# Performance work log

Hardware: AMD Instinct MI355X
Metric: run time of the kernel (lower is better)

Reference implementation:

```python
import jax, jax.numpy as jnp
import numpy as np

B, S, D, H = 2, 2048, 512, 8
DK = D // H
MASK_VALUE = -1e9


def setup_inputs() -> dict:
    key = jax.random.key(0)
    ks = jax.random.split(key, 12)
    scale = 1.0 / np.sqrt(D)
    inp = {
        "query": jax.random.normal(ks[0], (B, S, D), jnp.float32),
        "key": jax.random.normal(ks[1], (B, S, D), jnp.float32),
        "value": jax.random.normal(ks[2], (B, S, D), jnp.float32),
        # causal mask, broadcastable over batch and heads
        "mask": jnp.tril(jnp.ones((S, S), jnp.int32))[None, None, :, :],
        "Wq": jax.random.normal(ks[3], (D, D), jnp.float32) * scale,
        "bq": jax.random.normal(ks[4], (D,), jnp.float32) * scale,
        "Wk": jax.random.normal(ks[5], (D, D), jnp.float32) * scale,
        "bk": jax.random.normal(ks[6], (D,), jnp.float32) * scale,
        "Wv": jax.random.normal(ks[7], (D, D), jnp.float32) * scale,
        "bv": jax.random.normal(ks[8], (D,), jnp.float32) * scale,
        "Wo": jax.random.normal(ks[9], (D, D), jnp.float32) * scale,
        "bo": jax.random.normal(ks[10], (D,), jnp.float32) * scale,
    }
    return inp


def reference(query, key, value, mask, Wq, bq, Wk, bk, Wv, bv, Wo, bo):
    # linear projections (torch Linear: x @ W.T + b)
    q = query @ Wq.T + bq
    k = key @ Wk.T + bk
    v = value @ Wv.T + bv
    # split heads: [B,S,D] -> [B,H,S,DK]
    q = q.reshape(B, S, H, DK).transpose(0, 2, 1, 3)
    k = k.reshape(B, S, H, DK).transpose(0, 2, 1, 3)
    v = v.reshape(B, S, H, DK).transpose(0, 2, 1, 3)
    # scaled dot-product attention with explicit [B,H,S,S] score matrix
    scores = jnp.einsum("bhqd,bhkd->bhqk", q, k) / jnp.sqrt(jnp.float32(DK))
    scores = jnp.where(mask == 0, jnp.float32(MASK_VALUE), scores)
    attn = jax.nn.softmax(scores, axis=-1)
    x = jnp.einsum("bhqk,bhkd->bhqd", attn, v)
    # merge heads: [B,H,S,DK] -> [B,S,D]
    x = x.transpose(0, 2, 1, 3).reshape(B, S, D)
    return x @ Wo.T + bo
```

## Files before the change

### kernel.cpp

```cpp
#include <hip/hip_runtime.h>
#include <hip/hip_bf16.h>

#define B_   2
#define S_   2048
#define D_   512
#define H_   8
#define DK_  64
#define M_   (B_*S_)

typedef float  floatx4 __attribute__((ext_vector_type(4)));
typedef __bf16 bf16x8  __attribute__((ext_vector_type(8)));

#define MFMA16x16x32(a,b,c) __builtin_amdgcn_mfma_f32_16x16x32_bf16((a),(b),(c),0,0,0)

static __device__ __forceinline__ void load_lds16(const void* g, void* l) {
  __builtin_amdgcn_global_load_lds(
      (const __attribute__((address_space(1))) void*)g,
      (__attribute__((address_space(3))) void*)l,
      16, 0, 0);
}

static __device__ __forceinline__ bf16x8 cvt8(float4 a, float4 b) {
  bf16x8 r;
  r[0]=(__bf16)a.x; r[1]=(__bf16)a.y; r[2]=(__bf16)a.z; r[3]=(__bf16)a.w;
  r[4]=(__bf16)b.x; r[5]=(__bf16)b.y; r[6]=(__bf16)b.z; r[7]=(__bf16)b.w;
  return r;
}

static __device__ __forceinline__ int part_idx(int bh, int t, int s) {
  const int g = t >> 3;
  const int basec = (g == 2) ? 16 : ((g == 3) ? 40 : 0);
  return bh*72 + basec + (t - 8*g)*(g + 1) + s;
}


__global__ __launch_bounds__(256) void proj_qkv(
    const float* __restrict__ q_in, const float* __restrict__ k_in,
    const float* __restrict__ v_in,
    const float* __restrict__ Wq32, const float* __restrict__ Wk32,
    const float* __restrict__ Wv32,
    const float* __restrict__ bq, const float* __restrict__ bk,
    const float* __restrict__ bv,
    __bf16* __restrict__ Qb, __bf16* __restrict__ Kb, __bf16* __restrict__ Vtb)
{
  __shared__ __align__(16) __bf16 smem[16384];

  const int z = blockIdx.z;
  const float* X   = (z==0) ? q_in : (z==1) ? k_in : v_in;
  const float* W32 = (z==0) ? Wq32 : (z==1) ? Wk32 : Wv32;
  const float* bias = (z==0) ? bq : (z==1) ? bk : bv;

  const int m0 = blockIdx.x * 128;
  const int n0 = blockIdx.y * 128;
  const int tid  = threadIdx.x;
  const int w    = tid >> 6;
  const int lane = tid & 63;
  const int lcol = lane & 15;
  const int quad = lane >> 4;
  const int wm = w & 1, wn = w >> 1;

  const int uA0 = tid, uA1 = tid + 256;

  floatx4 zero = {0.f,0.f,0.f,0.f};
  floatx4 acc[4][4];
#pragma unroll
  for (int i = 0; i < 4; ++i)
#pragma unroll
    for (int nt = 0; nt < 4; ++nt) acc[i][nt] = zero;

  float4 a00,a01,a10,a11, b00,b01,b10,b11;
  auto ldAB = [&](int k0) {
    const float* pa0 = X   + (size_t)(m0 + (uA0 >> 2))*D_ + k0 + (uA0 & 3)*8;
    const float* pa1 = X   + (size_t)(m0 + (uA1 >> 2))*D_ + k0 + (uA1 & 3)*8;
    const float* pb0 = W32 + (size_t)(n0 + (uA0 >> 2))*D_ + k0 + (uA0 & 3)*8;
    const float* pb1 = W32 + (size_t)(n0 + (uA1 >> 2))*D_ + k0 + (uA1 & 3)*8;
    a00 = *(const float4*)pa0; a01 = *(const float4*)(pa0 + 4);
    a10 = *(const float4*)pa1; a11 = *(const float4*)(pa1 + 4);
    b00 = *(const float4*)pb0; b01 = *(const float4*)(pb0 + 4);
    b10 = *(const float4*)pb1; b11 = *(const float4*)(pb1 + 4);
  };
  auto wrAB = [&](int bsel) {
    *(bf16x8*)(smem + bsel*4096 + uA0*8)        = cvt8(a00, a01);
    *(bf16x8*)(smem + bsel*4096 + uA1*8)        = cvt8(a10, a11);
    *(bf16x8*)(smem + 8192 + bsel*4096 + uA0*8) = cvt8(b00, b01);
    *(bf16x8*)(smem + 8192 + bsel*4096 + uA1*8) = cvt8(b10, b11);
  };

  ldAB(0); wrAB(0);
  for (int it = 0; it < 16; ++it) {
    __syncthreads();
    const bool havenext = (it + 1 < 16);
    if (havenext) ldAB((it+1)*32);
    const __bf16* ab = smem + (it&1)*4096;
    const __bf16* bb = smem + 8192 + (it&1)*4096;
    bf16x8 af[4], bf[4];
#pragma unroll
    for (int i = 0; i < 4; ++i)
      af[i] = *(const bf16x8*)(ab + (wm*64 + i*16 + lcol)*32 + quad*8);
#pragma unroll
    for (int nt = 0; nt < 4; ++nt)
      bf[nt] = *(const bf16x8*)(bb + (wn*64 + nt*16 + lcol)*32 + quad*8);
#pragma unroll
    for (int i = 0; i < 4; ++i)
#pragma unroll
      for (int nt = 0; nt < 4; ++nt)
        acc[i][nt] = MFMA16x16x32(af[i], bf[nt], acc[i][nt]);
    if (havenext) wrAB((it+1)&1);
  }

  __syncthreads();
#pragma unroll
  for (int nt = 0; nt < 4; ++nt) {
    const int n = n0 + wn*64 + nt*16 + lcol;
    const float bias_n = bias[n];
    const int h_l = (n >> 6) & 1;
    const int dk  = n & 63;
#pragma unroll
    for (int i = 0; i < 4; ++i)
#pragma unroll
      for (int r = 0; r < 4; ++r) {
        const int m = m0 + wm*64 + i*16 + quad*4 + r;
        const float val = acc[i][nt][r] + bias_n;
        const int p = h_l*2 + ((m >> 6) & 1);
        const int klo = m & 63;
        int off;
        if (z == 0) {
          off = klo*64 + dk;
        } else if (z == 1) {
          off = (((klo>>4)*2 + (dk>>5))*64 + ((dk>>3)&3)*16 + (klo&15))*8 + (dk&7);
        } else {
          off = (((dk>>4)*2 + (klo>>5))*64 + ((klo>>3)&3)*16 + (dk&15))*8 + (klo&7);
        }
        smem[p*4096 + off] = (__bf16)val;
      }
  }
  __syncthreads();

  __bf16* dst = (z==0) ? Qb : (z==1) ? Kb : Vtb;
  const int bb2 = m0 >> 11;
  const int hh0 = n0 >> 6;
  const int cc0 = (m0 & 2047) >> 6;
#pragma unroll
  for (int it2 = 0; it2 < 8; ++it2) {
    const int u = it2*256 + tid;
    const int p = u >> 9, o = u & 511;
    const size_t base = ((size_t)(bb2*H_ + hh0 + (p>>1)))*(S_*DK_)
                      + (size_t)(cc0 + (p&1))*4096;
    *(bf16x8*)(dst + base + o*8) = *(const bf16x8*)(smem + p*4096 + o*8);
  }
}

__global__ __launch_bounds__(256) void attn_fwd(
    const __bf16* __restrict__ Qb, const __bf16* __restrict__ Kb,
    const __bf16* __restrict__ Vtb, __bf16* __restrict__ attnb,
    __bf16* __restrict__ Pb, float* __restrict__ Lb)
{
  __shared__ __align__(16) __bf16 kbuf[2][4096];
  __shared__ __align__(16) __bf16 vbuf[2][4096];
  __shared__ __align__(16) __bf16 pbuf[4][16*72];

  const int tid  = threadIdx.x;
  const int w    = tid >> 6;
  const int lane = tid & 63;
  const int lcol = lane & 15;
  const int quad = lane >> 4;
  const int hh = blockIdx.y;
  const int bb = blockIdx.z;

  const int wid = blockIdx.x;
  int t, s;
  if (wid < 8)       { t = wid;                  s = 0; }
  else if (wid < 24) { int u = wid - 8;  t = 8  + (u>>1); s = u & 1; }
  else if (wid < 48) { int u = wid - 24; int q3 = u/3; t = 16 + q3; s = u - 3*q3; }
  else               { int u = wid - 48; t = 24 + (u>>2); s = u & 3; }
  const bool single = (wid < 8);

  const int cbeg = s*8;
  const int cend = (cbeg + 8 < t + 1) ? (cbeg + 8) : (t + 1);
  const int q0  = t * 64;
  const int qr0 = q0 + w*16;

  const __bf16* Qp = Qb  + (size_t)(bb*H_ + hh) * S_ * DK_;
  const __bf16* Kp = Kb  + (size_t)(bb*H_ + hh) * S_ * DK_;
  const __bf16* Vp = Vtb + (size_t)(bb*H_ + hh) * DK_ * S_;

  const bf16x8 aq0 = *(const bf16x8*)(Qp + (size_t)(qr0 + lcol)*DK_ + quad*8);
  const bf16x8 aq1 = *(const bf16x8*)(Qp + (size_t)(qr0 + lcol)*DK_ + 32 + quad*8);

  floatx4 zero = {0.f,0.f,0.f,0.f};
  floatx4 acc[4] = {zero, zero, zero, zero};
  float lsum[4] = {0.f, 0.f, 0.f, 0.f};

  auto stage_chunk = [&](int bsel, int c) {
    const char* ksrc = (const char*)(Kp + (size_t)c * 4096);
    const char* vsrc = (const char*)(Vp + (size_t)c * 4096);
#pragma unroll
    for (int j = 0; j < 2; ++j) {
      const int off = w*2048 + j*1024;
      load_lds16(ksrc + off + lane*16, (char*)kbuf[bsel] + off);
      load_lds16(vsrc + off + lane*16, (char*)vbuf[bsel] + off);
    }
  };

  stage_chunk(0, cbeg);
  for (int c = cbeg; c < cend; ++c) {
    __syncthreads();
    if (c + 1 < cend) stage_chunk((c - cbeg + 1)&1, c+1);
    const int bsel = (c - cbeg) & 1;
    const int k0 = c * 64;
    const __bf16* kb = kbuf[bsel];
    const __bf16* vb = vbuf[bsel];

    floatx4 sc[4];
#pragma unroll
    for (int nt = 0; nt < 4; ++nt) {
      bf16x8 kf0 = *(const bf16x8*)(kb + (nt*2+0)*512 + lane*8);
      bf16x8 kf1 = *(const bf16x8*)(kb + (nt*2+1)*512 + lane*8);
      sc[nt] = MFMA16x16x32(aq1, kf1, MFMA16x16x32(aq0, kf0, zero));
    }

    const bool edge = (k0 + 63 > qr0);
#pragma unroll
    for (int nt = 0; nt < 4; ++nt) {
#pragma unroll
      for (int r = 0; r < 4; ++r) {
        float p = exp2f(sc[nt][r] * 0.18033688011112042f);
        if (edge) {
          const int qrow = qr0 + quad*4 + r;
          if (k0 + nt*16 + lcol > qrow) p = 0.f;
        }
        lsum[r] += p;
        pbuf[w][(quad*4 + r)*72 + nt*16 + lcol] = (__bf16)p;
      }
    }
    asm volatile("s_waitcnt lgkmcnt(0)" ::: "memory");

    const bf16x8 pa0 = *(const bf16x8*)(&pbuf[w][lcol*72 + quad*8]);
    const bf16x8 pa1 = *(const bf16x8*)(&pbuf[w][lcol*72 + 32 + quad*8]);
#pragma unroll
    for (int nt = 0; nt < 4; ++nt) {
      bf16x8 vf0 = *(const bf16x8*)(vb + (nt*2+0)*512 + lane*8);
      bf16x8 vf1 = *(const bf16x8*)(vb + (nt*2+1)*512 + lane*8);
      acc[nt] = MFMA16x16x32(pa0, vf0, acc[nt]);
      acc[nt] = MFMA16x16x32(pa1, vf1, acc[nt]);
    }
  }

  float tv[4];
#pragma unroll
  for (int r = 0; r < 4; ++r) {
    float v = lsum[r];
    v += __shfl_xor(v, 1, 16);
    v += __shfl_xor(v, 2, 16);
    v += __shfl_xor(v, 4, 16);
    v += __shfl_xor(v, 8, 16);
    tv[r] = v;
  }

  if (single) {
#pragma unroll
    for (int nt = 0; nt < 4; ++nt)
#pragma unroll
      for (int r = 0; r < 4; ++r) {
        const int q = qr0 + quad*4 + r;
        attnb[((size_t)(bb*S_ + q)) * D_ + hh*DK_ + nt*16 + lcol] =
            (__bf16)(acc[nt][r] / tv[r]);
      }
  } else {
    const int pidx = part_idx(bb*H_ + hh, t, s);
#pragma unroll
    for (int nt = 0; nt < 4; ++nt)
#pragma unroll
      for (int r = 0; r < 4; ++r)
        pbuf[w][(quad*4 + r)*72 + nt*16 + lcol] = (__bf16)acc[nt][r];
    asm volatile("s_waitcnt lgkmcnt(0)" ::: "memory");

    __bf16* pdst = Pb + (size_t)pidx*4096 + w*16*64;
#pragma unroll
    for (int i = 0; i < 2; ++i) {
      const int unit = i*64 + lane;
      const int row = unit >> 3, grp = unit & 7;
      *(bf16x8*)(pdst + row*64 + grp*8) =
          *(const bf16x8*)(&pbuf[w][row*72 + grp*8]);
    }
    if (lcol == 0) {
#pragma unroll
      for (int r = 0; r < 4; ++r)
        Lb[(size_t)pidx*64 + w*16 + quad*4 + r] = tv[r];
    }
  }
}

__global__ __launch_bounds__(256) void proj_out(
    const __bf16* __restrict__ attnb, const __bf16* __restrict__ Pb,
    const float* __restrict__ Lb, const float* __restrict__ Wo32,
    const float* __restrict__ bo, float* __restrict__ out)
{
  __shared__ __align__(16) __bf16 smem[12288];

  const int m0 = blockIdx.x * 64;
  const int n0 = blockIdx.y * 128;
  const int tid  = threadIdx.x;
  const int w    = tid >> 6;
  const int lane = tid & 63;
  const int lcol = lane & 15;
  const int quad = lane >> 4;
  const int wm = w & 1, wn = w >> 1;

  const int bb  = m0 >> 11;
  const int t   = (m0 & 2047) >> 6;
  const bool direct = (t < 8);
  const int g = t >> 3;
  const int nseg = g + 1;

  const int au  = tid;
  const int arow = au >> 2;
  const int ac8l = (au & 3) * 8;

  const int uB0 = tid, uB1 = tid + 256;

  floatx4 zero = {0.f,0.f,0.f,0.f};
  floatx4 acc[2][4];
#pragma unroll
  for (int i = 0; i < 2; ++i)
#pragma unroll
    for (int nt = 0; nt < 4; ++nt) acc[i][nt] = zero;

  float4 wb00, wb01, wb10, wb11;
  auto ldB = [&](int k0) {
    const float* p0 = Wo32 + (size_t)(n0 + (uB0 >> 2))*D_ + k0 + (uB0 & 3)*8;
    const float* p1 = Wo32 + (size_t)(n0 + (uB1 >> 2))*D_ + k0 + (uB1 & 3)*8;
    wb00 = *(const float4*)p0; wb01 = *(const float4*)(p0 + 4);
    wb10 = *(const float4*)p1; wb11 = *(const float4*)(p1 + 4);
  };
  auto wrB = [&](int bsel) {
    *(bf16x8*)(smem + 4096 + bsel*4096 + uB0*8) = cvt8(wb00, wb01);
    *(bf16x8*)(smem + 4096 + bsel*4096 + uB1*8) = cvt8(wb10, wb11);
  };
  auto stageA_direct = [&](int bsel, int k0) {
    load_lds16(attnb + (size_t)(m0 + arow)*D_ + k0 + ac8l,
               (char*)(smem + bsel*2048) + w*1024);
  };

  bf16x8 pv[4];
  float  pl[4];
  auto loadA_part = [&](int k0) {
    const int hh = k0 >> 6;
    const int cblk = k0 & 63;
    const int pidx0 = part_idx(bb*H_ + hh, t, 0);
#pragma unroll 4
    for (int s2 = 0; s2 < 4; ++s2) {
      if (s2 < nseg) {
        pv[s2] = *(const bf16x8*)(Pb + (size_t)(pidx0 + s2)*4096
                                   + arow*64 + cblk + ac8l);
        pl[s2] = Lb[(size_t)(pidx0 + s2)*64 + arow];
      }
    }
  };
  auto storeA_part = [&](int bsel) {
    float sum[8] = {0,0,0,0,0,0,0,0};
    float l = 0.f;
#pragma unroll 4
    for (int s2 = 0; s2 < 4; ++s2) {
      if (s2 < nseg) {
#pragma unroll
        for (int j = 0; j < 8; ++j) sum[j] += (float)pv[s2][j];
        l += pl[s2];
      }
    }
    const float rinv = 1.0f / l;
    bf16x8 o;
#pragma unroll
    for (int j = 0; j < 8; ++j) o[j] = (__bf16)(sum[j] * rinv);
    *(bf16x8*)(smem + bsel*2048 + au*8) = o;
  };

  ldB(0); wrB(0);
  if (direct) {
    stageA_direct(0, 0);
  } else {
    loadA_part(0);
    storeA_part(0);
  }

  for (int it = 0; it < 16; ++it) {
    __syncthreads();
    const bool havenext = (it + 1 < 16);
    if (havenext) {
      ldB((it+1)*32);
      if (direct) stageA_direct((it+1)&1, (it+1)*32);
      else        loadA_part((it+1)*32);
    }
    const __bf16* ab = smem + (it&1)*2048;
    const __bf16* bbp = smem + 4096 + (it&1)*4096;
    bf16x8 af[2], bf[4];
#pragma unroll
    for (int i = 0; i < 2; ++i)
      af[i] = *(const bf16x8*)(ab + (wm*32 + i*16 + lcol)*32 + quad*8);
#pragma unroll
    for (int nt = 0; nt < 4; ++nt)
      bf[nt] = *(const bf16x8*)(bbp + (wn*64 + nt*16 + lcol)*32 + quad*8);
#pragma unroll
    for (int i = 0; i < 2; ++i)
#pragma unroll
      for (int nt = 0; nt < 4; ++nt)
        acc[i][nt] = MFMA16x16x32(af[i], bf[nt], acc[i][nt]);
    if (havenext) {
      wrB((it+1)&1);
      if (!direct) storeA_part((it+1)&1);
    }
  }

#pragma unroll
  for (int nt = 0; nt < 4; ++nt) {
    const int n = n0 + wn*64 + nt*16 + lcol;
    const float bias_n = bo[n];
#pragma unroll
    for (int i = 0; i < 2; ++i)
#pragma unroll
      for (int r = 0; r < 4; ++r) {
        const int m = m0 + wm*32 + i*16 + quad*4 + r;
        out[(size_t)m * D_ + n] = acc[i][nt][r] + bias_n;
      }
  }
}

extern "C" void kernel_launch(void* const* d_in, const int* in_sizes, int n_in,
                              void* d_out, int out_size, void* d_ws, size_t ws_size,
                              hipStream_t stream) {
  const float* q_in = (const float*)d_in[0];
  const float* k_in = (const float*)d_in[1];
  const float* v_in = (const float*)d_in[2];
  const float* Wq = (const float*)d_in[4];
  const float* bq = (const float*)d_in[5];
  const float* Wk = (const float*)d_in[6];
  const float* bk = (const float*)d_in[7];
  const float* Wv = (const float*)d_in[8];
  const float* bv = (const float*)d_in[9];
  const float* Wo = (const float*)d_in[10];
  const float* bo = (const float*)d_in[11];
  float* out = (float*)d_out;

  __bf16* ws    = (__bf16*)d_ws;
  __bf16* Qb    = ws;
  __bf16* Kb    = ws + 1*2097152;
  __bf16* Vtb   = ws + 2*2097152;
  __bf16* attnb = ws + 3*2097152;
  __bf16* Pb    = ws + 4*2097152;
  float*  Lb    = (float*)(Pb + 1152*4096);

  proj_qkv<<<dim3(M_/128, D_/128, 3), dim3(256), 0, stream>>>(
      q_in, k_in, v_in, Wq, Wk, Wv, bq, bk, bv, Qb, Kb, Vtb);

  attn_fwd<<<dim3(80, H_, B_), dim3(256), 0, stream>>>(
      Qb, Kb, Vtb, attnb, Pb, Lb);

  proj_out<<<dim3(M_/64, D_/128), dim3(256), 0, stream>>>(
      attnb, Pb, Lb, Wo, bo, out);
}
```

Baseline: 168.3 us.

## Shrink projection tiles to 64x64, pad LDS rows, split-K output projection

```diff
diff --git a/kernel.cpp b/kernel.cpp
--- a/kernel.cpp
+++ b/kernel.cpp
@@ -12,6 +12,9 @@
 typedef __bf16 bf16x8  __attribute__((ext_vector_type(8)));
 
 #define MFMA16x16x32(a,b,c) __builtin_amdgcn_mfma_f32_16x16x32_bf16((a),(b),(c),0,0,0)
+
+#define PST 40
+#define PBUF 2560
 
 static __device__ __forceinline__ void load_lds16(const void* g, void* l) {
   __builtin_amdgcn_global_load_lds(
@@ -43,47 +46,36 @@
     const float* __restrict__ bv,
     __bf16* __restrict__ Qb, __bf16* __restrict__ Kb, __bf16* __restrict__ Vtb)
 {
-  __shared__ __align__(16) __bf16 smem[16384];
+  __shared__ __align__(16) __bf16 smem[4*PBUF];
 
   const int z = blockIdx.z;
-  const float* X   = (z==0) ? q_in : (z==1) ? k_in : v_in;
-  const float* W32 = (z==0) ? Wq32 : (z==1) ? Wk32 : Wv32;
+  const float* X    = (z==0) ? q_in : (z==1) ? k_in : v_in;
+  const float* W32  = (z==0) ? Wq32 : (z==1) ? Wk32 : Wv32;
   const float* bias = (z==0) ? bq : (z==1) ? bk : bv;
 
-  const int m0 = blockIdx.x * 128;
-  const int n0 = blockIdx.y * 128;
+  const int m0 = blockIdx.x * 64;
+  const int n0 = blockIdx.y * 64;
   const int tid  = threadIdx.x;
   const int w    = tid >> 6;
   const int lane = tid & 63;
   const int lcol = lane & 15;
   const int quad = lane >> 4;
-  const int wm = w & 1, wn = w >> 1;
-
-  const int uA0 = tid, uA1 = tid + 256;
+
+  const int arow = tid >> 2, ac = (tid & 3) * 8;
 
   floatx4 zero = {0.f,0.f,0.f,0.f};
-  floatx4 acc[4][4];
-#pragma unroll
-  for (int i = 0; i < 4; ++i)
-#pragma unroll
-    for (int nt = 0; nt < 4; ++nt) acc[i][nt] = zero;
-
-  float4 a00,a01,a10,a11, b00,b01,b10,b11;
+  floatx4 acc[4] = {zero, zero, zero, zero};
+
+  float4 a0,a1,b0,b1;
   auto ldAB = [&](int k0) {
-    const float* pa0 = X   + (size_t)(m0 + (uA0 >> 2))*D_ + k0 + (uA0 & 3)*8;
-    const float* pa1 = X   + (size_t)(m0 + (uA1 >> 2))*D_ + k0 + (uA1 & 3)*8;
-    const float* pb0 = W32 + (size_t)(n0 + (uA0 >> 2))*D_ + k0 + (uA0 & 3)*8;
-    const float* pb1 = W32 + (size_t)(n0 + (uA1 >> 2))*D_ + k0 + (uA1 & 3)*8;
-    a00 = *(const float4*)pa0; a01 = *(const float4*)(pa0 + 4);
-    a10 = *(const float4*)pa1; a11 = *(const float4*)(pa1 + 4);
-    b00 = *(const float4*)pb0; b01 = *(const float4*)(pb0 + 4);
-    b10 = *(const float4*)pb1; b11 = *(const float4*)(pb1 + 4);
+    const float* pa = X   + (size_t)(m0 + arow)*D_ + k0 + ac;
+    const float* pb = W32 + (size_t)(n0 + arow)*D_ + k0 + ac;
+    a0 = *(const float4*)pa; a1 = *(const float4*)(pa + 4);
+    b0 = *(const float4*)pb; b1 = *(const float4*)(pb + 4);
   };
   auto wrAB = [&](int bsel) {
-    *(bf16x8*)(smem + bsel*4096 + uA0*8)        = cvt8(a00, a01);
-    *(bf16x8*)(smem + bsel*4096 + uA1*8)        = cvt8(a10, a11);
-    *(bf16x8*)(smem + 8192 + bsel*4096 + uA0*8) = cvt8(b00, b01);
-    *(bf16x8*)(smem + 8192 + bsel*4096 + uA1*8) = cvt8(b10, b11);
+    *(bf16x8*)(smem + bsel*PBUF + arow*PST + ac)         = cvt8(a0, a1);
+    *(bf16x8*)(smem + 2*PBUF + bsel*PBUF + arow*PST + ac) = cvt8(b0, b1);
   };
 
   ldAB(0); wrAB(0);
@@ -91,62 +83,50 @@
     __syncthreads();
     const bool havenext = (it + 1 < 16);
     if (havenext) ldAB((it+1)*32);
-    const __bf16* ab = smem + (it&1)*4096;
-    const __bf16* bb = smem + 8192 + (it&1)*4096;
-    bf16x8 af[4], bf[4];
-#pragma unroll
-    for (int i = 0; i < 4; ++i)
-      af[i] = *(const bf16x8*)(ab + (wm*64 + i*16 + lcol)*32 + quad*8);
-#pragma unroll
-    for (int nt = 0; nt < 4; ++nt)
-      bf[nt] = *(const bf16x8*)(bb + (wn*64 + nt*16 + lcol)*32 + quad*8);
-#pragma unroll
-    for (int i = 0; i < 4; ++i)
-#pragma unroll
-      for (int nt = 0; nt < 4; ++nt)
-        acc[i][nt] = MFMA16x16x32(af[i], bf[nt], acc[i][nt]);
+    const __bf16* ab = smem + (it&1)*PBUF;
+    const __bf16* bb = smem + 2*PBUF + (it&1)*PBUF;
+    const bf16x8 af = *(const bf16x8*)(ab + (w*16 + lcol)*PST + quad*8);
+    bf16x8 bf[4];
+#pragma unroll
+    for (int nt = 0; nt < 4; ++nt)
+      bf[nt] = *(const bf16x8*)(bb + (nt*16 + lcol)*PST + quad*8);
+#pragma unroll
+    for (int nt = 0; nt < 4; ++nt)
+      acc[nt] = MFMA16x16x32(af, bf[nt], acc[nt]);
     if (havenext) wrAB((it+1)&1);
   }
 
   __syncthreads();
 #pragma unroll
   for (int nt = 0; nt < 4; ++nt) {
-    const int n = n0 + wn*64 + nt*16 + lcol;
-    const float bias_n = bias[n];
-    const int h_l = (n >> 6) & 1;
-    const int dk  = n & 63;
-#pragma unroll
-    for (int i = 0; i < 4; ++i)
-#pragma unroll
-      for (int r = 0; r < 4; ++r) {
-        const int m = m0 + wm*64 + i*16 + quad*4 + r;
-        const float val = acc[i][nt][r] + bias_n;
-        const int p = h_l*2 + ((m >> 6) & 1);
-        const int klo = m & 63;
-        int off;
-        if (z == 0) {
-          off = klo*64 + dk;
-        } else if (z == 1) {
-          off = (((klo>>4)*2 + (dk>>5))*64 + ((dk>>3)&3)*16 + (klo&15))*8 + (dk&7);
-        } else {
-          off = (((dk>>4)*2 + (klo>>5))*64 + ((klo>>3)&3)*16 + (dk&15))*8 + (klo&7);
-        }
-        smem[p*4096 + off] = (__bf16)val;
-      }
+    const int dk = nt*16 + lcol;
+    const float bias_n = bias[n0 + dk];
+#pragma unroll
+    for (int r = 0; r < 4; ++r) {
+      const int klo = w*16 + quad*4 + r;
+      const float val = acc[nt][r] + bias_n;
+      int off;
+      if (z == 0) {
+        off = klo*64 + dk;
+      } else if (z == 1) {
+        off = (((klo>>4)*2 + (dk>>5))*64 + ((dk>>3)&3)*16 + (klo&15))*8 + (dk&7);
+      } else {
+        off = (((dk>>4)*2 + (klo>>5))*64 + ((klo>>3)&3)*16 + (dk&15))*8 + (klo&7);
+      }
+      smem[off] = (__bf16)val;
+    }
   }
   __syncthreads();
 
   __bf16* dst = (z==0) ? Qb : (z==1) ? Kb : Vtb;
   const int bb2 = m0 >> 11;
-  const int hh0 = n0 >> 6;
-  const int cc0 = (m0 & 2047) >> 6;
-#pragma unroll
-  for (int it2 = 0; it2 < 8; ++it2) {
-    const int u = it2*256 + tid;
-    const int p = u >> 9, o = u & 511;
-    const size_t base = ((size_t)(bb2*H_ + hh0 + (p>>1)))*(S_*DK_)
-                      + (size_t)(cc0 + (p&1))*4096;
-    *(bf16x8*)(dst + base + o*8) = *(const bf16x8*)(smem + p*4096 + o*8);
+  const int hh  = n0 >> 6;
+  const int cch = (m0 & 2047) >> 6;
+  const size_t base = ((size_t)(bb2*H_ + hh))*(S_*DK_) + (size_t)cch*4096;
+#pragma unroll
+  for (int i = 0; i < 2; ++i) {
+    const int u = i*256 + tid;
+    *(bf16x8*)(dst + base + u*8) = *(const bf16x8*)(smem + u*8);
   }
 }
 
@@ -291,137 +271,124 @@
   }
 }
 
-__global__ __launch_bounds__(256) void proj_out(
+__global__ __launch_bounds__(512) void proj_out(
     const __bf16* __restrict__ attnb, const __bf16* __restrict__ Pb,
     const float* __restrict__ Lb, const float* __restrict__ Wo32,
     const float* __restrict__ bo, float* __restrict__ out)
 {
-  __shared__ __align__(16) __bf16 smem[12288];
+  __shared__ __align__(16) __bf16 smem[8*PBUF];
 
   const int m0 = blockIdx.x * 64;
-  const int n0 = blockIdx.y * 128;
+  const int n0 = blockIdx.y * 64;
   const int tid  = threadIdx.x;
+  const int g    = tid >> 8;
+  const int gt   = tid & 255;
   const int w    = tid >> 6;
+  const int wg   = w & 3;
   const int lane = tid & 63;
   const int lcol = lane & 15;
   const int quad = lane >> 4;
-  const int wm = w & 1, wn = w >> 1;
 
   const int bb  = m0 >> 11;
   const int t   = (m0 & 2047) >> 6;
   const bool direct = (t < 8);
-  const int g = t >> 3;
-  const int nseg = g + 1;
-
-  const int au  = tid;
-  const int arow = au >> 2;
-  const int ac8l = (au & 3) * 8;
-
-  const int uB0 = tid, uB1 = tid + 256;
+  const int nseg = (t >> 3) + 1;
+
+  const int arow = gt >> 2, ac = (gt & 3) * 8;
 
   floatx4 zero = {0.f,0.f,0.f,0.f};
-  floatx4 acc[2][4];
-#pragma unroll
-  for (int i = 0; i < 2; ++i)
-#pragma unroll
-    for (int nt = 0; nt < 4; ++nt) acc[i][nt] = zero;
-
-  float4 wb00, wb01, wb10, wb11;
+  floatx4 acc[4] = {zero, zero, zero, zero};
+
+  bf16x8 av;
+  bf16x8 pv[4]; float pl[4];
+  float4 wb0, wb1;
+
+  auto ldA = [&](int k0) {
+    if (direct) {
+      av = *(const bf16x8*)(attnb + (size_t)(m0 + arow)*D_ + k0 + ac);
+    } else {
+      const int hh = k0 >> 6;
+      const int cblk = k0 & 63;
+      const int pidx0 = part_idx(bb*H_ + hh, t, 0);
+#pragma unroll 4
+      for (int s2 = 0; s2 < 4; ++s2) {
+        if (s2 < nseg) {
+          pv[s2] = *(const bf16x8*)(Pb + (size_t)(pidx0 + s2)*4096
+                                     + arow*64 + cblk + ac);
+          pl[s2] = Lb[(size_t)(pidx0 + s2)*64 + arow];
+        }
+      }
+    }
+  };
   auto ldB = [&](int k0) {
-    const float* p0 = Wo32 + (size_t)(n0 + (uB0 >> 2))*D_ + k0 + (uB0 & 3)*8;
-    const float* p1 = Wo32 + (size_t)(n0 + (uB1 >> 2))*D_ + k0 + (uB1 & 3)*8;
-    wb00 = *(const float4*)p0; wb01 = *(const float4*)(p0 + 4);
-    wb10 = *(const float4*)p1; wb11 = *(const float4*)(p1 + 4);
-  };
-  auto wrB = [&](int bsel) {
-    *(bf16x8*)(smem + 4096 + bsel*4096 + uB0*8) = cvt8(wb00, wb01);
-    *(bf16x8*)(smem + 4096 + bsel*4096 + uB1*8) = cvt8(wb10, wb11);
-  };
-  auto stageA_direct = [&](int bsel, int k0) {
-    load_lds16(attnb + (size_t)(m0 + arow)*D_ + k0 + ac8l,
-               (char*)(smem + bsel*2048) + w*1024);
-  };
-
-  bf16x8 pv[4];
-  float  pl[4];
-  auto loadA_part = [&](int k0) {
-    const int hh = k0 >> 6;
-    const int cblk = k0 & 63;
-    const int pidx0 = part_idx(bb*H_ + hh, t, 0);
+    const float* pb = Wo32 + (size_t)(n0 + arow)*D_ + k0 + ac;
+    wb0 = *(const float4*)pb; wb1 = *(const float4*)(pb + 4);
+  };
+  auto wrAB = [&](int bsel) {
+    bf16x8 a;
+    if (direct) {
+      a = av;
+    } else {
+      float sum[8] = {0,0,0,0,0,0,0,0};
+      float l = 0.f;
 #pragma unroll 4
-    for (int s2 = 0; s2 < 4; ++s2) {
-      if (s2 < nseg) {
-        pv[s2] = *(const bf16x8*)(Pb + (size_t)(pidx0 + s2)*4096
-                                   + arow*64 + cblk + ac8l);
-        pl[s2] = Lb[(size_t)(pidx0 + s2)*64 + arow];
-      }
-    }
-  };
-  auto storeA_part = [&](int bsel) {
-    float sum[8] = {0,0,0,0,0,0,0,0};
-    float l = 0.f;
-#pragma unroll 4
-    for (int s2 = 0; s2 < 4; ++s2) {
-      if (s2 < nseg) {
-#pragma unroll
-        for (int j = 0; j < 8; ++j) sum[j] += (float)pv[s2][j];
-        l += pl[s2];
-      }
-    }
-    const float rinv = 1.0f / l;
-    bf16x8 o;
-#pragma unroll
-    for (int j = 0; j < 8; ++j) o[j] = (__bf16)(sum[j] * rinv);
-    *(bf16x8*)(smem + bsel*2048 + au*8) = o;
-  };
-
-  ldB(0); wrB(0);
-  if (direct) {
-    stageA_direct(0, 0);
-  } else {
-    loadA_part(0);
-    storeA_part(0);
-  }
-
-  for (int it = 0; it < 16; ++it) {
+      for (int s2 = 0; s2 < 4; ++s2) {
+        if (s2 < nseg) {
+#pragma unroll
+          for (int j = 0; j < 8; ++j) sum[j] += (float)pv[s2][j];
+          l += pl[s2];
+        }
+      }
+      const float rinv = 1.0f / l;
+#pragma unroll
+      for (int j = 0; j < 8; ++j) a[j] = (__bf16)(sum[j] * rinv);
+    }
+    *(bf16x8*)(smem + (g*2 + bsel)*PBUF + arow*PST + ac) = a;
+    *(bf16x8*)(smem + 4*PBUF + (g*2 + bsel)*PBUF + arow*PST + ac)
+        = cvt8(wb0, wb1);
+  };
+
+  const int kbase = g * 256;
+  ldA(kbase); ldB(kbase); wrAB(0);
+  for (int it = 0; it < 8; ++it) {
     __syncthreads();
-    const bool havenext = (it + 1 < 16);
-    if (havenext) {
-      ldB((it+1)*32);
-      if (direct) stageA_direct((it+1)&1, (it+1)*32);
-      else        loadA_part((it+1)*32);
-    }
-    const __bf16* ab = smem + (it&1)*2048;
-    const __bf16* bbp = smem + 4096 + (it&1)*4096;
-    bf16x8 af[2], bf[4];
-#pragma unroll
-    for (int i = 0; i < 2; ++i)
-      af[i] = *(const bf16x8*)(ab + (wm*32 + i*16 + lcol)*32 + quad*8);
-#pragma unroll
-    for (int nt = 0; nt < 4; ++nt)
-      bf[nt] = *(const bf16x8*)(bbp + (wn*64 + nt*16 + lcol)*32 + quad*8);
-#pragma unroll
-    for (int i = 0; i < 2; ++i)
-#pragma unroll
-      for (int nt = 0; nt < 4; ++nt)
-        acc[i][nt] = MFMA16x16x32(af[i], bf[nt], acc[i][nt]);
-    if (havenext) {
-      wrB((it+1)&1);
-      if (!direct) storeA_part((it+1)&1);
-    }
-  }
-
-#pragma unroll
-  for (int nt = 0; nt < 4; ++nt) {
-    const int n = n0 + wn*64 + nt*16 + lcol;
-    const float bias_n = bo[n];
-#pragma unroll
-    for (int i = 0; i < 2; ++i)
+    const bool havenext = (it + 1 < 8);
+    if (havenext) { ldA(kbase + (it+1)*32); ldB(kbase + (it+1)*32); }
+    const __bf16* ab = smem + (g*2 + (it&1))*PBUF;
+    const __bf16* bbp = smem + 4*PBUF + (g*2 + (it&1))*PBUF;
+    const bf16x8 af = *(const bf16x8*)(ab + (wg*16 + lcol)*PST + quad*8);
+    bf16x8 bf[4];
+#pragma unroll
+    for (int nt = 0; nt < 4; ++nt)
+      bf[nt] = *(const bf16x8*)(bbp + (nt*16 + lcol)*PST + quad*8);
+#pragma unroll
+    for (int nt = 0; nt < 4; ++nt)
+      acc[nt] = MFMA16x16x32(af, bf[nt], acc[nt]);
+    if (havenext) wrAB((it+1)&1);
+  }
+
+  __syncthreads();
+  float* fbuf = (float*)smem;
+  if (g == 1) {
+#pragma unroll
+    for (int nt = 0; nt < 4; ++nt)
+#pragma unroll
+      for (int r = 0; r < 4; ++r)
+        fbuf[(wg*16 + quad*4 + r)*68 + nt*16 + lcol] = acc[nt][r];
+  }
+  __syncthreads();
+  if (g == 0) {
+#pragma unroll
+    for (int nt = 0; nt < 4; ++nt) {
+      const int n = n0 + nt*16 + lcol;
+      const float bias_n = bo[n];
 #pragma unroll
       for (int r = 0; r < 4; ++r) {
-        const int m = m0 + wm*32 + i*16 + quad*4 + r;
-        out[(size_t)m * D_ + n] = acc[i][nt][r] + bias_n;
-      }
+        const int row = wg*16 + quad*4 + r;
+        const float val = acc[nt][r] + fbuf[row*68 + nt*16 + lcol] + bias_n;
+        out[(size_t)(m0 + row) * D_ + n] = val;
+      }
+    }
   }
 }
 
@@ -449,12 +416,12 @@
   __bf16* Pb    = ws + 4*2097152;
   float*  Lb    = (float*)(Pb + 1152*4096);
 
-  proj_qkv<<<dim3(M_/128, D_/128, 3), dim3(256), 0, stream>>>(
+  proj_qkv<<<dim3(M_/64, D_/64, 3), dim3(256), 0, stream>>>(
       q_in, k_in, v_in, Wq, Wk, Wv, bq, bk, bv, Qb, Kb, Vtb);
 
   attn_fwd<<<dim3(80, H_, B_), dim3(256), 0, stream>>>(
       Qb, Kb, Vtb, attnb, Pb, Lb);
 
-  proj_out<<<dim3(M_/64, D_/128), dim3(256), 0, stream>>>(
+  proj_out<<<dim3(M_/64, D_/64), dim3(512), 0, stream>>>(
       attnb, Pb, Lb, Wo, bo, out);
 }
```

Measured after the change: 162.7 us. 1.03x faster.
